# Kernel tuning notes

Hardware: AMD Instinct MI355X
Metric: run time of the kernel (lower is better)

The kernel has to match this reference:

```python
import jax, jax.numpy as jnp
import numpy as np

B, F, U = 16384, 64, 64  # batch, in_features, num_units per FeatureNN

# FeatureNN per the NAM paper / reproduced-nam repo: one ExU layer with ReLU-1
# activation -> linear projection to a scalar. ExU: h = relu_n((x - b) * exp(w)),
# n = 1 (clip at 1). Dropout / feature_dropout are identity at inference (p=0).

def setup_inputs() -> dict:
    key = jax.random.key(0)
    k1, k2, k3, k4, k5 = jax.random.split(key, 5)
    inputs = jax.random.normal(k1, (B, F), dtype=jnp.float32)
    # Per-feature ExU params, stacked over the feature axis so all F tiny MLPs
    # run as one batched op (block-diagonal view of the Python loop).
    exu_w = jax.random.normal(k2, (F, U), dtype=jnp.float32) * 0.5  # exp(w) weights
    exu_b = jax.random.normal(k3, (F,), dtype=jnp.float32) * 0.5    # ExU bias (shift)
    lin_w = jax.random.normal(k4, (F, U), dtype=jnp.float32) * (1.0 / np.sqrt(U))
    lin_b = jax.random.normal(k5, (F,), dtype=jnp.float32) * 0.01
    bias = jnp.zeros((1,), dtype=jnp.float32)  # global NAM bias
    return {"inputs": inputs, "exu_w": exu_w, "exu_b": exu_b,
            "lin_w": lin_w, "lin_b": lin_b, "bias": bias}


def reference(inputs, exu_w, exu_b, lin_w, lin_b, bias):
    # ExU unit over all features at once: (B,F,1) -> (B,F,U)
    h = (inputs[:, :, None] - exu_b[None, :, None]) * jnp.exp(exu_w)[None]
    h = jnp.clip(jax.nn.relu(h), 0.0, 1.0)  # ReLU-1
    # Per-feature linear head to scalar: (B,F,U) x (F,U) -> (B,F)
    fnn_out = jnp.einsum('bfu,fu->bf', h, lin_w) + lin_b[None, :]
    # feature_dropout is identity (p=0 at inference)
    out = fnn_out.sum(axis=-1) + bias[0]  # (B,)
    return out, fnn_out
```

## Files before the change

### kernel.cpp

```cpp
#include <hip/hip_runtime.h>


#define NB 16384
#define NF 64
#define NU 64
#define LDS_P 65

__global__ __launch_bounds__(256, 2) void nam_reg(
    const float* __restrict__ x,
    const float* __restrict__ exu_w,
    const float* __restrict__ exu_b,
    const float* __restrict__ lin_w,
    const float* __restrict__ lin_b,
    const float* __restrict__ bias,
    float* __restrict__ out,
    float* __restrict__ fnn) {

    __shared__ float ews[NF * LDS_P];
    __shared__ float lws[NF * LDS_P];

    const int t = threadIdx.x;
    const int lane = t & 63;
    const int wid = (blockIdx.x * 256 + t) >> 6;

#pragma unroll
    for (int k = 0; k < 4; ++k) {
        int g = (k * 256 + t) * 4;
        float4 a = *(const float4*)(exu_w + g);
        float4 b = *(const float4*)(lin_w + g);
        int f = g >> 6;
        int u = g & 63;
        float* ep = &ews[f * LDS_P + u];
        float* lp = &lws[f * LDS_P + u];
        ep[0] = __expf(a.x); ep[1] = __expf(a.y);
        ep[2] = __expf(a.z); ep[3] = __expf(a.w);
        lp[0] = b.x; lp[1] = b.y; lp[2] = b.z; lp[3] = b.w;
    }

    const float eb = exu_b[lane];
    const float lb = lin_b[lane];
    const float b0 = bias[0];

    __syncthreads();

    float ew[NU], lw[NU];
#pragma unroll
    for (int u = 0; u < NU; ++u) {
        ew[u] = ews[lane * LDS_P + u];
        lw[u] = lws[lane * LDS_P + u];
    }

    const int rbase = wid * 8;
#pragma unroll
    for (int rq = 0; rq < 2; ++rq) {
        const int r = rbase + rq * 4;

        float xv0 = x[(size_t)(r + 0) * NF + lane] - eb;
        float xv1 = x[(size_t)(r + 1) * NF + lane] - eb;
        float xv2 = x[(size_t)(r + 2) * NF + lane] - eb;
        float xv3 = x[(size_t)(r + 3) * NF + lane] - eb;

        float a0 = 0.f, a1 = 0.f, a2 = 0.f, a3 = 0.f;
#pragma unroll
        for (int u = 0; u < NU; ++u) {
            const float e = ew[u], w = lw[u];
            a0 = __builtin_fmaf(__builtin_amdgcn_fmed3f(xv0 * e, 0.f, 1.f), w, a0);
            a1 = __builtin_fmaf(__builtin_amdgcn_fmed3f(xv1 * e, 0.f, 1.f), w, a1);
            a2 = __builtin_fmaf(__builtin_amdgcn_fmed3f(xv2 * e, 0.f, 1.f), w, a2);
            a3 = __builtin_fmaf(__builtin_amdgcn_fmed3f(xv3 * e, 0.f, 1.f), w, a3);
        }
        a0 += lb; a1 += lb; a2 += lb; a3 += lb;

        fnn[(size_t)(r + 0) * NF + lane] = a0;
        fnn[(size_t)(r + 1) * NF + lane] = a1;
        fnn[(size_t)(r + 2) * NF + lane] = a2;
        fnn[(size_t)(r + 3) * NF + lane] = a3;

        float s0 = a0, s1 = a1, s2 = a2, s3 = a3;
#pragma unroll
        for (int m = 1; m < 64; m <<= 1) {
            s0 += __shfl_xor(s0, m, 64);
            s1 += __shfl_xor(s1, m, 64);
            s2 += __shfl_xor(s2, m, 64);
            s3 += __shfl_xor(s3, m, 64);
        }
        if (lane == 0) {
            *(float4*)(out + r) = make_float4(s0 + b0, s1 + b0, s2 + b0, s3 + b0);
        }
    }
}

extern "C" void kernel_launch(void* const* d_in, const int* in_sizes, int n_in,
                              void* d_out, int out_size, void* d_ws, size_t ws_size,
                              hipStream_t stream) {
    const float* x     = (const float*)d_in[0];
    const float* exu_w = (const float*)d_in[1];
    const float* exu_b = (const float*)d_in[2];
    const float* lin_w = (const float*)d_in[3];
    const float* lin_b = (const float*)d_in[4];
    const float* bias  = (const float*)d_in[5];

    float* out = (float*)d_out;
    float* fnn = out + NB;

    nam_reg<<<dim3(512), dim3(256), 0, stream>>>(
        x, exu_w, exu_b, lin_w, lin_b, bias, out, fnn);
}
```

Measured before the change: 12.01 us.

## Fold exp weights into linear weights and clamp against reciprocal bound

Rewrites relu1(x*e)*w as (w*e)*clamp(x, 0, 1/e), so each inner-loop element becomes one med3 and one FMA with no multiply. The per-feature constants are precomputed in LDS with float4 stores and loads at padding 68. All 8 rows are processed at once to give more independent accumulators and batch the shuffle reductions. This relies on the hardware reciprocal approximation and changes rounding slightly. It also raises register pressure with 8 inputs and 8 accumulators live.

```diff
diff --git a/kernel.cpp b/kernel.cpp
--- a/kernel.cpp
+++ b/kernel.cpp
@@ -4,7 +4,7 @@
 #define NB 16384
 #define NF 64
 #define NU 64
-#define LDS_P 65
+#define LDP 68
 
 __global__ __launch_bounds__(256, 2) void nam_reg(
     const float* __restrict__ x,
@@ -16,8 +16,8 @@
     float* __restrict__ out,
     float* __restrict__ fnn) {
 
-    __shared__ float ews[NF * LDS_P];
-    __shared__ float lws[NF * LDS_P];
+    __shared__ float pws[NF * LDP];
+    __shared__ float qws[NF * LDP];
 
     const int t = threadIdx.x;
     const int lane = t & 63;
@@ -30,11 +30,12 @@
         float4 b = *(const float4*)(lin_w + g);
         int f = g >> 6;
         int u = g & 63;
-        float* ep = &ews[f * LDS_P + u];
-        float* lp = &lws[f * LDS_P + u];
-        ep[0] = __expf(a.x); ep[1] = __expf(a.y);
-        ep[2] = __expf(a.z); ep[3] = __expf(a.w);
-        lp[0] = b.x; lp[1] = b.y; lp[2] = b.z; lp[3] = b.w;
+        float e0 = __expf(a.x), e1 = __expf(a.y), e2 = __expf(a.z), e3 = __expf(a.w);
+        *(float4*)&pws[f * LDP + u] = make_float4(b.x * e0, b.y * e1, b.z * e2, b.w * e3);
+        *(float4*)&qws[f * LDP + u] = make_float4(__builtin_amdgcn_rcpf(e0),
+                                                  __builtin_amdgcn_rcpf(e1),
+                                                  __builtin_amdgcn_rcpf(e2),
+                                                  __builtin_amdgcn_rcpf(e3));
     }
 
     const float eb = exu_b[lane];
@@ -43,50 +44,51 @@
 
     __syncthreads();
 
-    float ew[NU], lw[NU];
+    float p[NU], q[NU];
+    {
+        const float4* pr = (const float4*)&pws[lane * LDP];
+        const float4* qr = (const float4*)&qws[lane * LDP];
 #pragma unroll
-    for (int u = 0; u < NU; ++u) {
-        ew[u] = ews[lane * LDS_P + u];
-        lw[u] = lws[lane * LDS_P + u];
+        for (int k = 0; k < NU / 4; ++k) {
+            float4 pv = pr[k];
+            float4 qv = qr[k];
+            p[4*k+0] = pv.x; p[4*k+1] = pv.y; p[4*k+2] = pv.z; p[4*k+3] = pv.w;
+            q[4*k+0] = qv.x; q[4*k+1] = qv.y; q[4*k+2] = qv.z; q[4*k+3] = qv.w;
+        }
     }
 
     const int rbase = wid * 8;
+    float xv[8], acc[8];
 #pragma unroll
-    for (int rq = 0; rq < 2; ++rq) {
-        const int r = rbase + rq * 4;
+    for (int j = 0; j < 8; ++j) {
+        xv[j] = x[(size_t)(rbase + j) * NF + lane] - eb;
+        acc[j] = 0.0f;
+    }
 
-        float xv0 = x[(size_t)(r + 0) * NF + lane] - eb;
-        float xv1 = x[(size_t)(r + 1) * NF + lane] - eb;
-        float xv2 = x[(size_t)(r + 2) * NF + lane] - eb;
-        float xv3 = x[(size_t)(r + 3) * NF + lane] - eb;
+#pragma unroll
+    for (int u = 0; u < NU; ++u) {
+        const float pu = p[u], qu = q[u];
+#pragma unroll
+        for (int j = 0; j < 8; ++j) {
+            acc[j] = __builtin_fmaf(pu, __builtin_amdgcn_fmed3f(xv[j], 0.f, qu), acc[j]);
+        }
+    }
 
-        float a0 = 0.f, a1 = 0.f, a2 = 0.f, a3 = 0.f;
+    float s[8];
 #pragma unroll
-        for (int u = 0; u < NU; ++u) {
-            const float e = ew[u], w = lw[u];
-            a0 = __builtin_fmaf(__builtin_amdgcn_fmed3f(xv0 * e, 0.f, 1.f), w, a0);
-            a1 = __builtin_fmaf(__builtin_amdgcn_fmed3f(xv1 * e, 0.f, 1.f), w, a1);
-            a2 = __builtin_fmaf(__builtin_amdgcn_fmed3f(xv2 * e, 0.f, 1.f), w, a2);
-            a3 = __builtin_fmaf(__builtin_amdgcn_fmed3f(xv3 * e, 0.f, 1.f), w, a3);
-        }
-        a0 += lb; a1 += lb; a2 += lb; a3 += lb;
-
-        fnn[(size_t)(r + 0) * NF + lane] = a0;
-        fnn[(size_t)(r + 1) * NF + lane] = a1;
-        fnn[(size_t)(r + 2) * NF + lane] = a2;
-        fnn[(size_t)(r + 3) * NF + lane] = a3;
-
-        float s0 = a0, s1 = a1, s2 = a2, s3 = a3;
+    for (int j = 0; j < 8; ++j) {
+        float a = acc[j] + lb;
+        fnn[(size_t)(rbase + j) * NF + lane] = a;
+        s[j] = a;
+    }
 #pragma unroll
-        for (int m = 1; m < 64; m <<= 1) {
-            s0 += __shfl_xor(s0, m, 64);
-            s1 += __shfl_xor(s1, m, 64);
-            s2 += __shfl_xor(s2, m, 64);
-            s3 += __shfl_xor(s3, m, 64);
-        }
-        if (lane == 0) {
-            *(float4*)(out + r) = make_float4(s0 + b0, s1 + b0, s2 + b0, s3 + b0);
-        }
+    for (int m = 1; m < 64; m <<= 1) {
+#pragma unroll
+        for (int j = 0; j < 8; ++j) s[j] += __shfl_xor(s[j], m, 64);
+    }
+    if (lane == 0) {
+        *(float4*)(out + rbase)     = make_float4(s[0] + b0, s[1] + b0, s[2] + b0, s[3] + b0);
+        *(float4*)(out + rbase + 4) = make_float4(s[4] + b0, s[5] + b0, s[6] + b0, s[7] + b0);
     }
 }
 
```

Result: faster. 11.24 us (-6.4%).
